# Performance work log

Measured on AMD Instinct MI355X. Metric: run time of the kernel, lower is better.

The kernel has to match this reference:

```python
import jax, jax.numpy as jnp
import numpy as np

V, E, H = 50000, 128, 256  # vocab, embedding_size, hidden_size
S, B = 512, 64             # seq_len, batch (seq-first, torch LSTM default)


def setup_inputs() -> dict:
    key = jax.random.key(0)
    ks = jax.random.split(key, 10)
    u = 1.0 / np.sqrt(H)  # torch LSTM/Linear init bound

    def unif(k, sh):
        return jax.random.uniform(k, sh, jnp.float32, -u, u)

    emb = jax.random.normal(ks[0], (V, E), jnp.float32) * 0.02
    emb = emb.at[0].set(0.0)  # padding_idx=0

    inp = {
        "seq": jax.random.randint(ks[1], (S, B), 0, V),
        "emb": emb,
        # forward direction weights (gate order i,f,g,o like torch)
        "W_ih_f": unif(ks[2], (4 * H, E)),
        "W_hh_f": unif(ks[3], (4 * H, H)),
        "b_f": unif(ks[4], (4 * H,)),  # b_ih + b_hh fused (identical math)
        # reverse direction
        "W_ih_b": unif(ks[5], (4 * H, E)),
        "W_hh_b": unif(ks[6], (4 * H, H)),
        "b_b": unif(ks[7], (4 * H,)),
        # classification head over concatenated bi-directional features
        "W_out": unif(ks[8], (1, 2 * H)),
        "b_out": unif(ks[9], (1,)),
    }
    return inp


def _lstm_scan(xg, W_hh):
    """xg: [S,B,4H] precomputed input-gate projections; returns hidden seq [S,B,H]."""
    b = xg.shape[1]
    h0 = jnp.zeros((b, H), xg.dtype)
    c0 = jnp.zeros((b, H), xg.dtype)

    def step(carry, xg_t):
        h, c = carry
        gates = xg_t + h @ W_hh.T  # [B,4H]
        i, f, g, o = jnp.split(gates, 4, axis=-1)
        i = jax.nn.sigmoid(i)
        f = jax.nn.sigmoid(f)
        g = jnp.tanh(g)
        o = jax.nn.sigmoid(o)
        c = f * c + i * g
        h = o * jnp.tanh(c)
        return (h, c), h

    _, hs = jax.lax.scan(step, (h0, c0), xg)
    return hs


def reference(seq, emb, W_ih_f, W_hh_f, b_f, W_ih_b, W_hh_b, b_b, W_out, b_out):
    # embedding with padding_idx=0 (row 0 contributes zero)
    x = jnp.where((seq == 0)[..., None], 0.0, emb[seq])  # [S,B,E]

    xg_f = jnp.einsum("sbe,ge->sbg", x, W_ih_f) + b_f          # [S,B,4H]
    hs_f = _lstm_scan(xg_f, W_hh_f)                             # [S,B,H]

    xr = x[::-1]
    xg_b = jnp.einsum("sbe,ge->sbg", xr, W_ih_b) + b_b
    hs_b = _lstm_scan(xg_b, W_hh_b)[::-1]                       # [S,B,H]

    out = jnp.concatenate([hs_f, hs_b], axis=-1)                # [S,B,2H]
    last = out[-1]                                              # [B,2H]
    return jax.nn.sigmoid(last @ W_out.T + b_out)               # [B,1]
```

## Files before the change

### kernel.cpp

```cpp
#include <hip/hip_runtime.h>
#include <hip/hip_bf16.h>
#include <stdint.h>
#include <string.h>

#define S_LEN 512
#define NBATCH 64
#define EDIM 128
#define HDIM 256
#define GDIM 1024

#define WQ_SCALE 1024.0f
#define HQ_SCALE 127.0f
#define LOG2E 1.4426950408889634f
#define C_IFO (-1.1093545e-05f)
#define C_G (2.2187090e-05f)

typedef __attribute__((ext_vector_type(8))) short short8;
typedef __attribute__((ext_vector_type(4))) short short4v;
typedef __attribute__((ext_vector_type(4))) float float4v;
typedef __attribute__((ext_vector_type(4))) int int4v;

#define OFF_WHH8 0u
#define SZ_WHH8 (256u * 64u * 16u)
#define OFF_WIH (OFF_WHH8 + SZ_WHH8)
#define SZ_WIH (64u * 4u * 64u * 16u)
#define OFF_XG ((size_t)(OFF_WIH + SZ_WIH))
#define SZ_XG ((size_t)S_LEN * NBATCH * GDIM * 2)
#define OFF_HF (OFF_XG + SZ_XG)

__device__ __forceinline__ short f2bf(float f) {
    union { float f; unsigned u; } v;
    v.f = f;
    unsigned r = (v.u + 0x7fffu + ((v.u >> 16) & 1u)) >> 16;
    return (short)r;
}
__device__ __forceinline__ float bf2f(short s) {
    union { unsigned u; float f; } v;
    v.u = ((unsigned)(unsigned short)s) << 16;
    return v.f;
}
__device__ __forceinline__ float sigm(float x) {
    float e = __expf(-x);
    return __builtin_amdgcn_rcpf(1.0f + e);
}
__device__ __forceinline__ float tanh_(float x) {
    float e = __expf(2.0f * x);
    return 1.0f - 2.0f * __builtin_amdgcn_rcpf(e + 1.0f);
}

__global__ __launch_bounds__(256) void prep_frags(const float* __restrict__ src,
                                                  char* __restrict__ dst,
                                                  int K, int nchunks, int nfrags) {
    int id = blockIdx.x * blockDim.x + threadIdx.x;
    int lane = id & 63;
    int f = id >> 6;
    if (f >= nfrags) return;
    int tile = f / nchunks;
    int c = f - tile * nchunks;
    int row = tile * 16 + (lane & 15);
    int k0 = c * 32 + ((lane >> 4) * 8);
    const float* s = src + (size_t)row * K + k0;
    short8 pack;
#pragma unroll
    for (int j = 0; j < 8; ++j) pack[j] = f2bf(s[j]);
    *(short8*)(dst + ((size_t)f * 64 + lane) * 16) = pack;
}

__global__ __launch_bounds__(256) void prep_whh_i8(const float* __restrict__ src,
                                                   char* __restrict__ dst) {
    int id = blockIdx.x * blockDim.x + threadIdx.x;
    int lane = id & 63;
    int f = id >> 6;
    int tile = f >> 2, kc = f & 3;
    int row = tile * 16 + (lane & 15);
    int k0 = kc * 64 + ((lane >> 4) * 16);
    const float* s = src + (size_t)row * HDIM + k0;
    union { char b[16]; int4v v; } u;
#pragma unroll
    for (int b = 0; b < 16; ++b)
        u.b[b] = (char)(int)rintf(s[b] * WQ_SCALE);
    *(int4v*)(dst + ((size_t)f * 64 + lane) * 16) = u.v;
}

__global__ __launch_bounds__(256) void input_proj(const int* __restrict__ seq,
                                                  const float* __restrict__ emb,
                                                  const char* __restrict__ wih_frags,
                                                  const float* __restrict__ bias,
                                                  char* __restrict__ xg) {
    __shared__ __align__(16) short lx[4][16][136];
    int tid = threadIdx.x;
    int t0 = blockIdx.x * 4;
    int g = blockIdx.y;

    {
        int row = tid >> 2;
        int tt = row >> 4, m = row & 15;
        int k0 = (tid & 3) * 32;
        int v = seq[(t0 + tt) * NBATCH + g * 16 + m];
        const float* src = emb + (size_t)v * EDIM + k0;
        bool zero = (v == 0);
#pragma unroll
        for (int u = 0; u < 32; u += 4) {
            float4v f = *(const float4v*)(src + u);
            short4v p;
#pragma unroll
            for (int e = 0; e < 4; ++e) p[e] = zero ? (short)0 : f2bf(f[e]);
            *(short4v*)&lx[tt][m][k0 + u] = p;
        }
    }
    __syncthreads();

    int lane = tid & 63, w = tid >> 6;
    int ln = lane & 15, q = lane >> 4;

    short8 Bx[4][4];
#pragma unroll
    for (int tt = 0; tt < 4; ++tt)
#pragma unroll
        for (int c = 0; c < 4; ++c)
            Bx[tt][c] = *(const short8*)&lx[tt][ln][c * 32 + q * 8];

    for (int nt = 0; nt < 16; ++nt) {
        int tile = w * 16 + nt;
        float kg = ((tile >> 4) == 2) ? (2.0f * LOG2E) : (-LOG2E);
        short8 Aw[4];
#pragma unroll
        for (int c = 0; c < 4; ++c)
            Aw[c] = *(const short8*)(wih_frags + (((size_t)tile * 4 + c) * 64 + lane) * 16);
        float4v b4 = *(const float4v*)(bias + tile * 16 + q * 4);
#pragma unroll
        for (int tt = 0; tt < 4; ++tt) {
            float4v acc = b4;
#pragma unroll
            for (int c = 0; c < 4; ++c)
                acc = __builtin_amdgcn_mfma_f32_16x16x32_bf16(Aw[c], Bx[tt][c], acc, 0, 0, 0);
            short4v p;
#pragma unroll
            for (int r = 0; r < 4; ++r) p[r] = f2bf(acc[r] * kg);
            size_t off = ((size_t)(t0 + tt) * NBATCH + g * 16 + ln) * GDIM + tile * 16 + q * 4;
            *(short4v*)(xg + off * 2) = p;
        }
    }
}

__global__ __launch_bounds__(512, 2) void lstm_scan(const char* __restrict__ whh8,
                                                    const char* __restrict__ xg,
                                                    float* __restrict__ hf_out) {
    __shared__ __align__(16) char hls[2][16][272];
    __shared__ __align__(16) int scr[8][256];
    int tid = threadIdx.x;
    int lane = tid & 63, w = tid >> 6;
    int ln = lane & 15, q = lane >> 4;
    int bg = blockIdx.x;

    int4v Wfr[4][2][4];
#pragma unroll
    for (int g = 0; g < 4; ++g)
#pragma unroll
        for (int p = 0; p < 2; ++p) {
            int tile = g * 16 + (w * 2 + p);
#pragma unroll
            for (int kc = 0; kc < 4; ++kc)
                Wfr[g][p][kc] = *(const int4v*)(whh8 + (((size_t)(tile * 4 + kc)) * 64 + lane) * 16);
        }

    {
        int* hp = (int*)&hls[0][0][0];
        for (int i = tid; i < (2 * 16 * 272) / 4; i += 512) hp[i] = 0;
    }

    const char* hrd = &hls[0][0][0];
    char* hwr = &hls[1][0][0];
    int hoff_rd = ln * 272 + q * 16;

    int b = ln & 1;
    int rr = (ln >> 1) & 3;
    int p = ln >> 3;
    int j = (w * 2 + p) * 16 + q * 4 + rr;
    int hoff_wr = b * 272 + j;

    int* swr = &scr[w][0];
    const int* srd = &scr[w][0] + (q * 16 + p * 8 + b * 4 + rr);

    float cst = 0.0f;

    const char* xgp = xg + (((size_t)(bg * 2 + b) * GDIM + j) * 2);
    const size_t tstep = (size_t)NBATCH * GDIM * 2;

    unsigned short xq[4];
#pragma unroll
    for (int g = 0; g < 4; ++g)
        xq[g] = *(const unsigned short*)(xgp + g * 512);

    __syncthreads();

    const int4v z4 = {0, 0, 0, 0};
    for (int t = 0; t < S_LEN; ++t) {
        int4v Bh[4];
#pragma unroll
        for (int kc = 0; kc < 4; ++kc)
            Bh[kc] = *(const int4v*)(hrd + hoff_rd + kc * 64);

        float xgf[4];
#pragma unroll
        for (int g = 0; g < 4; ++g) xgf[g] = bf2f((short)xq[g]);
        xgp += tstep;
        if (t != S_LEN - 1) {
#pragma unroll
            for (int g = 0; g < 4; ++g)
                xq[g] = *(const unsigned short*)(xgp + g * 512);
        }

        int4v a[4][2];
#pragma unroll
        for (int g = 0; g < 4; ++g)
#pragma unroll
            for (int pp = 0; pp < 2; ++pp)
                a[g][pp] = __builtin_amdgcn_mfma_i32_16x16x64_i8(Wfr[g][pp][0], Bh[0], z4, 0, 0, 0);
#pragma unroll
        for (int kc = 1; kc < 4; ++kc)
#pragma unroll
            for (int g = 0; g < 4; ++g)
#pragma unroll
                for (int pp = 0; pp < 2; ++pp)
                    a[g][pp] = __builtin_amdgcn_mfma_i32_16x16x64_i8(Wfr[g][pp][kc], Bh[kc], a[g][pp], 0, 0, 0);

        if (ln < 2) {
#pragma unroll
            for (int g = 0; g < 4; ++g)
#pragma unroll
                for (int pp = 0; pp < 2; ++pp)
                    *(int4v*)(swr + g * 64 + q * 16 + pp * 8 + ln * 4) = a[g][pp];
        }
        float s0 = fmaf((float)srd[0], C_IFO, xgf[0]);
        float s1 = fmaf((float)srd[64], C_IFO, xgf[1]);
        float s2 = fmaf((float)srd[128], C_G, xgf[2]);
        float s3 = fmaf((float)srd[192], C_IFO, xgf[3]);

        float iv = __builtin_amdgcn_rcpf(1.0f + exp2f(s0));
        float fv = __builtin_amdgcn_rcpf(1.0f + exp2f(s1));
        float gv = fmaf(-2.0f, __builtin_amdgcn_rcpf(1.0f + exp2f(s2)), 1.0f);
        float ov = __builtin_amdgcn_rcpf(1.0f + exp2f(s3));
        float cv = fmaf(fv, cst, iv * gv);
        cst = cv;
        float tc = fmaf(-2.0f, __builtin_amdgcn_rcpf(1.0f + exp2f(cv * (2.0f * LOG2E))), 1.0f);
        float hv = ov * tc;

        int hq = (int)rintf(hv * HQ_SCALE);
        hwr[hoff_wr] = (char)hq;

        if (t == S_LEN - 1)
            hf_out[((size_t)(bg * 2 + b)) * HDIM + j] = hv;

        const char* tr = hrd; hrd = hwr; hwr = (char*)tr;
        __syncthreads();
    }
}

__global__ __launch_bounds__(256) void tail_kernel(const int* __restrict__ seq,
                                                   const float* __restrict__ emb,
                                                   const float* __restrict__ wih_b,
                                                   const float* __restrict__ b_b,
                                                   const float* __restrict__ wout,
                                                   const float* __restrict__ b_out,
                                                   const float* __restrict__ hf,
                                                   float* __restrict__ out) {
    __shared__ float xs[EDIM];
    __shared__ float red[4];
    int b = blockIdx.x, tid = threadIdx.x;
    if (tid < EDIM) {
        int v = seq[(S_LEN - 1) * NBATCH + b];
        xs[tid] = (v == 0) ? 0.0f : emb[(size_t)v * EDIM + tid];
    }
    __syncthreads();

    int j = tid;
    float si = b_b[j], sg = b_b[2 * HDIM + j], so = b_b[3 * HDIM + j];
    const float* wi = wih_b + (size_t)j * EDIM;
    const float* wg = wih_b + (size_t)(2 * HDIM + j) * EDIM;
    const float* wo = wih_b + (size_t)(3 * HDIM + j) * EDIM;
#pragma unroll 8
    for (int k = 0; k < EDIM; k += 4) {
        float4v x4 = *(const float4v*)&xs[k];
        float4v a = *(const float4v*)(wi + k);
        float4v c = *(const float4v*)(wg + k);
        float4v d = *(const float4v*)(wo + k);
#pragma unroll
        for (int e = 0; e < 4; ++e) {
            si += a[e] * x4[e];
            sg += c[e] * x4[e];
            so += d[e] * x4[e];
        }
    }
    float cc = sigm(si) * tanh_(sg);
    float hb = sigm(so) * tanh_(cc);
    float partial = hf[(size_t)b * HDIM + j] * wout[j] + hb * wout[HDIM + j];

    float val = partial;
#pragma unroll
    for (int off = 32; off > 0; off >>= 1) val += __shfl_down(val, off, 64);
    int lane = tid & 63, wv = tid >> 6;
    if (lane == 0) red[wv] = val;
    __syncthreads();
    if (tid == 0) out[b] = sigm(red[0] + red[1] + red[2] + red[3] + b_out[0]);
}

extern "C" void kernel_launch(void* const* d_in, const int* in_sizes, int n_in,
                              void* d_out, int out_size, void* d_ws, size_t ws_size,
                              hipStream_t stream) {
    const int* seq = (const int*)d_in[0];
    const float* emb = (const float*)d_in[1];
    const float* Wih_f = (const float*)d_in[2];
    const float* Whh_f = (const float*)d_in[3];
    const float* b_f = (const float*)d_in[4];
    const float* Wih_b = (const float*)d_in[5];
    const float* b_b = (const float*)d_in[7];
    const float* Wout = (const float*)d_in[8];
    const float* b_out = (const float*)d_in[9];
    float* out = (float*)d_out;
    char* ws = (char*)d_ws;

    prep_whh_i8<<<dim3(64), 256, 0, stream>>>(Whh_f, ws + OFF_WHH8);
    prep_frags<<<dim3(64), 256, 0, stream>>>(Wih_f, ws + OFF_WIH, EDIM, 4, 64 * 4);
    input_proj<<<dim3(S_LEN / 4, 4), 256, 0, stream>>>(seq, emb, ws + OFF_WIH, b_f, ws + OFF_XG);
    lstm_scan<<<dim3(32), 512, 0, stream>>>(ws + OFF_WHH8, ws + OFF_XG, (float*)(ws + OFF_HF));
    tail_kernel<<<dim3(NBATCH), 256, 0, stream>>>(seq, emb, Wih_b, b_b, Wout, b_out,
                                                  (const float*)(ws + OFF_HF), out);
}
```

Measured before the change: 723.0 us.

## Repartition LSTM scan: 16 warps per block, 4 batches per block

Measured after the change: 704.1 us. 1.03x faster.

```diff
diff --git a/kernel.cpp b/kernel.cpp
--- a/kernel.cpp
+++ b/kernel.cpp
@@ -143,48 +143,46 @@
     }
 }
 
-__global__ __launch_bounds__(512, 2) void lstm_scan(const char* __restrict__ whh8,
-                                                    const char* __restrict__ xg,
-                                                    float* __restrict__ hf_out) {
-    __shared__ __align__(16) char hls[2][16][272];
-    __shared__ __align__(16) int scr[8][256];
+#define HPAD 320
+__global__ __launch_bounds__(1024, 4) void lstm_scan(const char* __restrict__ whh8,
+                                                     const char* __restrict__ xg,
+                                                     float* __restrict__ hf_out) {
+    __shared__ __align__(16) char hls[2][4][HPAD];
+    __shared__ __align__(16) int scr[16][256];
     int tid = threadIdx.x;
     int lane = tid & 63, w = tid >> 6;
     int ln = lane & 15, q = lane >> 4;
     int bg = blockIdx.x;
 
-    int4v Wfr[4][2][4];
-#pragma unroll
-    for (int g = 0; g < 4; ++g)
-#pragma unroll
-        for (int p = 0; p < 2; ++p) {
-            int tile = g * 16 + (w * 2 + p);
-#pragma unroll
-            for (int kc = 0; kc < 4; ++kc)
-                Wfr[g][p][kc] = *(const int4v*)(whh8 + (((size_t)(tile * 4 + kc)) * 64 + lane) * 16);
-        }
+    int4v Wfr[4][4];
+#pragma unroll
+    for (int g = 0; g < 4; ++g) {
+        int tile = g * 16 + w;
+#pragma unroll
+        for (int kc = 0; kc < 4; ++kc)
+            Wfr[g][kc] = *(const int4v*)(whh8 + (((size_t)(tile * 4 + kc)) * 64 + lane) * 16);
+    }
 
     {
         int* hp = (int*)&hls[0][0][0];
-        for (int i = tid; i < (2 * 16 * 272) / 4; i += 512) hp[i] = 0;
+        for (int i = tid; i < (2 * 4 * HPAD) / 4; i += 1024) hp[i] = 0;
     }
 
     const char* hrd = &hls[0][0][0];
     char* hwr = &hls[1][0][0];
-    int hoff_rd = ln * 272 + q * 16;
-
-    int b = ln & 1;
-    int rr = (ln >> 1) & 3;
-    int p = ln >> 3;
-    int j = (w * 2 + p) * 16 + q * 4 + rr;
-    int hoff_wr = b * 272 + j;
-
-    int* swr = &scr[w][0];
-    const int* srd = &scr[w][0] + (q * 16 + p * 8 + b * 4 + rr);
+    int hoff_rd = (ln & 3) * HPAD + q * 16;
+
+    int b = ln & 3;
+    int rr = ln >> 2;
+    int j = w * 16 + q * 4 + rr;
+    int hoff_wr = b * HPAD + j;
+
+    int* swr = &scr[w][q * 16 + ln * 4];
+    const int* srd = &scr[w][q * 16 + b * 4 + rr];
 
     float cst = 0.0f;
 
-    const char* xgp = xg + (((size_t)(bg * 2 + b) * GDIM + j) * 2);
+    const char* xgp = xg + (((size_t)(bg * 4 + b) * GDIM + j) * 2);
     const size_t tstep = (size_t)NBATCH * GDIM * 2;
 
     unsigned short xq[4];
@@ -211,26 +209,20 @@
                 xq[g] = *(const unsigned short*)(xgp + g * 512);
         }
 
-        int4v a[4][2];
+        int4v a[4];
 #pragma unroll
         for (int g = 0; g < 4; ++g)
-#pragma unroll
-            for (int pp = 0; pp < 2; ++pp)
-                a[g][pp] = __builtin_amdgcn_mfma_i32_16x16x64_i8(Wfr[g][pp][0], Bh[0], z4, 0, 0, 0);
+            a[g] = __builtin_amdgcn_mfma_i32_16x16x64_i8(Wfr[g][0], Bh[0], z4, 0, 0, 0);
 #pragma unroll
         for (int kc = 1; kc < 4; ++kc)
 #pragma unroll
             for (int g = 0; g < 4; ++g)
-#pragma unroll
-                for (int pp = 0; pp < 2; ++pp)
-                    a[g][pp] = __builtin_amdgcn_mfma_i32_16x16x64_i8(Wfr[g][pp][kc], Bh[kc], a[g][pp], 0, 0, 0);
-
-        if (ln < 2) {
+                a[g] = __builtin_amdgcn_mfma_i32_16x16x64_i8(Wfr[g][kc], Bh[kc], a[g], 0, 0, 0);
+
+        if (ln < 4) {
 #pragma unroll
             for (int g = 0; g < 4; ++g)
-#pragma unroll
-                for (int pp = 0; pp < 2; ++pp)
-                    *(int4v*)(swr + g * 64 + q * 16 + pp * 8 + ln * 4) = a[g][pp];
+                *(int4v*)(swr + g * 64) = a[g];
         }
         float s0 = fmaf((float)srd[0], C_IFO, xgf[0]);
         float s1 = fmaf((float)srd[64], C_IFO, xgf[1]);
@@ -250,7 +242,7 @@
         hwr[hoff_wr] = (char)hq;
 
         if (t == S_LEN - 1)
-            hf_out[((size_t)(bg * 2 + b)) * HDIM + j] = hv;
+            hf_out[((size_t)(bg * 4 + b)) * HDIM + j] = hv;
 
         const char* tr = hrd; hrd = hwr; hwr = (char*)tr;
         __syncthreads();
@@ -323,7 +315,7 @@
     prep_whh_i8<<<dim3(64), 256, 0, stream>>>(Whh_f, ws + OFF_WHH8);
     prep_frags<<<dim3(64), 256, 0, stream>>>(Wih_f, ws + OFF_WIH, EDIM, 4, 64 * 4);
     input_proj<<<dim3(S_LEN / 4, 4), 256, 0, stream>>>(seq, emb, ws + OFF_WIH, b_f, ws + OFF_XG);
-    lstm_scan<<<dim3(32), 512, 0, stream>>>(ws + OFF_WHH8, ws + OFF_XG, (float*)(ws + OFF_HF));
+    lstm_scan<<<dim3(16), 1024, 0, stream>>>(ws + OFF_WHH8, ws + OFF_XG, (float*)(ws + OFF_HF));
     tail_kernel<<<dim3(NBATCH), 256, 0, stream>>>(seq, emb, Wih_b, b_b, Wout, b_out,
                                                   (const float*)(ws + OFF_HF), out);
 }
```
